# Performance work log

Hardware: AMD Instinct MI355X
Metric: run time of the kernel (lower is better)

Reference implementation:

```python
import jax, jax.numpy as jnp
import numpy as np

N_EDGES = 8_388_608      # total synapses (flat weight vector length)
NUM_TYPES = 200          # number of unique edge types (ragged groups)
STRENGTH = 1e-3          # regularizer strength (cast to float32 as in the TF module)


def setup_inputs() -> dict:
    key = jax.random.key(0)
    k1, k2, k3 = jax.random.split(key, 3)
    # Edges pre-sorted by edge type -> contiguous segments (equivalent to the
    # RaggedTensor.from_value_rowids grouping built in __init__).
    segment_ids = jnp.sort(
        jax.random.randint(k1, (N_EDGES,), 0, NUM_TYPES, dtype=jnp.int32))
    x = jax.random.normal(k2, (N_EDGES,), dtype=jnp.float32)
    init_raw = jax.random.normal(k3, (N_EDGES,), dtype=jnp.float32)
    # __init__ sorts the initial weights within each edge-type group; since
    # segment_ids is already sorted, lexsort with segment_ids as the primary
    # key sorts values within each contiguous segment.
    order = jnp.lexsort((init_raw, segment_ids))
    initial_sorted = init_raw[order]
    return {"x": x, "initial_sorted": initial_sorted, "segment_ids": segment_ids}


def reference(x, initial_sorted, segment_ids):
    x = x.astype(jnp.float32)
    # Segmented sort of the current weights: primary key = edge type,
    # secondary key = value. Equivalent to tf.sort(x_i) per ragged group.
    order = jnp.lexsort((x, segment_ids))
    x_sorted = x[order]                       # [n_edges], sorted within each group
    diff = jnp.abs(x_sorted - initial_sorted)  # per-edge |sorted(x) - sorted(y)|
    sums = jax.ops.segment_sum(diff, segment_ids, num_segments=NUM_TYPES)
    counts = jax.ops.segment_sum(jnp.ones_like(diff), segment_ids,
                                 num_segments=NUM_TYPES)
    emd = sums / jnp.maximum(counts, 1.0)      # per-group Wasserstein-1 (mean L1)
    return jnp.mean(emd) * jnp.float32(STRENGTH)
```

## Files before the change

kernel.cpp:

```cpp
#include <hip/hip_runtime.h>
#include <hip/hip_bf16.h>

#define NSEG 200
#define STRENGTH 1e-3f
#define NFB 16384
#define FSCALE (16384.0f / 12.0f)
#define BT 1024
#define SPLIT 5
#define WINCAP 9728
#define EPT 10
#define PSTRIDE (NFB + 8)
#define PCH 8192
#define SLICE_E 8200

__device__ __forceinline__ int fbin_of(float v) {
    float t = (v + 6.0f) * FSCALE;
    int b = (int)floorf(t);
    return b < 0 ? 0 : (b > NFB - 1 ? NFB - 1 : b);
}

__global__ void __launch_bounds__(BT)
k_hist(const float* __restrict__ x, const int* __restrict__ seg,
       int* __restrict__ seg_starts, float* __restrict__ segSums,
       unsigned* __restrict__ gcur, unsigned short* __restrict__ pfxg,
       int* __restrict__ Bg, int* __restrict__ Bpos, int N) {
    __shared__ unsigned hw[NFB / 2];
    __shared__ unsigned wsum[16];
    __shared__ int sh2[3];
    int s = blockIdx.x;
    int t = threadIdx.x;
    if (t <= 1) {
        int key = s + t;
        int lo = 0, hi = N;
        while (lo < hi) { int mid = (lo + hi) >> 1; if (seg[mid] < key) lo = mid + 1; else hi = mid; }
        sh2[t] = lo;
    }
    if (t < 8) gcur[s * 8 + t] = 0u;
    if (t == 2) segSums[s] = 0.f;
    for (int k = t; k < NFB / 2; k += BT) hw[k] = 0;
    __syncthreads();
    int st = sh2[0], en = sh2[1];
    if (t == 3) { seg_starts[s] = st; if (s == NSEG - 1) seg_starts[NSEG] = N; }
    int n = en - st;
    const float* xs = x + st;
    if (n > 0) {
        int head = min(n, (int)((4 - (st & 3)) & 3));
        for (int k = t; k < head; k += BT) { int f = fbin_of(xs[k]); atomicAdd(&hw[f >> 1], 1u << ((f & 1) * 16)); }
        int nv = (n - head) >> 2;
        const float4* xs4 = (const float4*)(xs + head);
        for (int j = t; j < nv; j += BT) {
            float4 v = xs4[j];
            int f0 = fbin_of(v.x), f1 = fbin_of(v.y), f2 = fbin_of(v.z), f3 = fbin_of(v.w);
            atomicAdd(&hw[f0 >> 1], 1u << ((f0 & 1) * 16));
            atomicAdd(&hw[f1 >> 1], 1u << ((f1 & 1) * 16));
            atomicAdd(&hw[f2 >> 1], 1u << ((f2 & 1) * 16));
            atomicAdd(&hw[f3 >> 1], 1u << ((f3 & 1) * 16));
        }
        for (int k = head + nv * 4 + t; k < n; k += BT) { int f = fbin_of(xs[k]); atomicAdd(&hw[f >> 1], 1u << ((f & 1) * 16)); }
    }
    __syncthreads();
    unsigned wv[8]; unsigned run = 0;
    #pragma unroll
    for (int i = 0; i < 8; ++i) {
        unsigned w = hw[t * 8 + i];
        unsigned c0 = w & 0xffffu, c1 = w >> 16;
        wv[i] = run | ((run + c0) << 16);
        run += c0 + c1;
    }
    unsigned incl = run;
    for (int off = 1; off < 64; off <<= 1) {
        unsigned nv2 = __shfl_up(incl, off, 64);
        if ((t & 63) >= off) incl += nv2;
    }
    if ((t & 63) == 63) wsum[t >> 6] = incl;
    __syncthreads();
    unsigned wb = 0; int myw = t >> 6;
    #pragma unroll
    for (int j = 0; j < 16; ++j) wb += (j < myw) ? wsum[j] : 0u;
    unsigned base = wb + incl - run;
    unsigned bb = base | (base << 16);
    unsigned short* pp = pfxg + (size_t)s * PSTRIDE;
    #pragma unroll
    for (int i = 0; i < 8; ++i) {
        unsigned pw = wv[i] + bb;
        hw[t * 8 + i] = pw;
        ((unsigned*)pp)[t * 8 + i] = pw;
    }
    if (t == BT - 1) { pp[NFB] = (unsigned short)(base + run); sh2[2] = (int)(base + run); }
    __syncthreads();
    int nsh = sh2[2];
    if (t == 0) { Bg[s * 8 + 0] = 0; Bg[s * 8 + SPLIT] = NFB; Bpos[s * 8 + 0] = 0; Bpos[s * 8 + SPLIT] = nsh; }
    if (t >= 1 && t < SPLIT) {
        int target = (int)(((long)t * nsh) / SPLIT);
        int lo = 0, hi = NFB - 1;
        while (lo < hi) {
            int mid = (lo + hi) >> 1;
            int pv = (int)((hw[(mid + 1) >> 1] >> (((mid + 1) & 1) * 16)) & 0xffffu);
            if (pv > target) hi = mid; else lo = mid + 1;
        }
        Bg[s * 8 + t] = lo;
        Bpos[s * 8 + t] = (int)((hw[lo >> 1] >> ((lo & 1) * 16)) & 0xffffu);
    }
}

__global__ void __launch_bounds__(1024)
k_part(const float* __restrict__ x, const int* __restrict__ seg_starts,
       const int* __restrict__ Bg, const int* __restrict__ Bpos,
       unsigned* __restrict__ gcur, float* __restrict__ part, int N) {
    __shared__ int sst[NSEG + 1];
    __shared__ unsigned hh[16][12];
    __shared__ int gb[10];
    __shared__ int sB[8];
    int t = threadIdx.x;
    for (int k = t; k < NSEG + 1; k += 1024) sst[k] = seg_starts[k];
    if (t < 192) ((unsigned*)hh)[t] = 0u;
    __syncthreads();
    int base = blockIdx.x * PCH;
    if (base >= N) return;
    int lo = 0, hi = NSEG - 1;
    while (lo < hi) { int mid = (lo + hi) >> 1; if (base < sst[mid + 1]) hi = mid; else lo = mid + 1; }
    int s0 = lo, bnd = sst[s0 + 1];
    if (t < 4) sB[t] = Bg[s0 * 8 + 1 + t];
    else if (t < 8) sB[t] = (s0 + 1 < NSEG) ? Bg[(s0 + 1) * 8 + 1 + (t - 4)] : 0x7fffffff;
    __syncthreads();
    int grp = t >> 6;
    float vv[8]; unsigned pk[8];
    const float4* x4 = (const float4*)(x + base);
    #pragma unroll
    for (int it = 0; it < 2; ++it) {
        int j = it * 1024 + t;
        int gi = base + j * 4;
        float4 v4 = (gi + 3 < N) ? x4[j] : make_float4(0.f, 0.f, 0.f, 0.f);
        #pragma unroll
        for (int e = 0; e < 4; ++e) {
            int i = it * 4 + e;
            float v = (e == 0) ? v4.x : (e == 1) ? v4.y : (e == 2) ? v4.z : v4.w;
            vv[i] = v;
            int g = gi + e;
            if (g < N) {
                int off = (g >= bnd) ? 4 : 0;
                int f = fbin_of(v);
                int p = (f >= sB[off]) + (f >= sB[off + 1]) + (f >= sB[off + 2]) + (f >= sB[off + 3]);
                int sp = (off >> 2) * 5 + p;
                unsigned lr = atomicAdd(&hh[grp][sp], 1u);
                pk[i] = ((unsigned)sp << 10) | lr;
            } else pk[i] = 0xffffffffu;
        }
    }
    __syncthreads();
    if (t < 10) {
        unsigned run = 0;
        #pragma unroll
        for (int g = 0; g < 16; ++g) { unsigned c = hh[g][t]; hh[g][t] = run; run += c; }
        int s = s0 + (t >= 5);
        int p = (t >= 5) ? t - 5 : t;
        int rsv = 0;
        if (run > 0 && s < NSEG) rsv = (int)atomicAdd(&gcur[s * 8 + p], run);
        gb[t] = (s < NSEG) ? (sst[s] + Bpos[s * 8 + p] + rsv) : 0;
    }
    __syncthreads();
    #pragma unroll
    for (int i = 0; i < 8; ++i) {
        if (pk[i] == 0xffffffffu) continue;
        int sp = (int)(pk[i] >> 10);
        int lr = (int)(pk[i] & 1023u);
        part[gb[sp] + (int)hh[grp][sp] + lr] = vv[i];
    }
}

__global__ void __launch_bounds__(BT)
k_seg(const float* __restrict__ part, const float* __restrict__ y,
      const int* __restrict__ seg_starts, const unsigned short* __restrict__ pfxg,
      const int* __restrict__ Bg, float* __restrict__ segSums) {
    __shared__ unsigned short slice[SLICE_E];
    __shared__ unsigned cur[2056];
    __shared__ __align__(16) float win[WINCAP + 4];
    __shared__ float warr[16];
    int s = blockIdx.x % NSEG;
    int p = blockIdx.x / NSEG;
    int t = threadIdx.x;
    int st = seg_starts[s], en = seg_starts[s + 1];
    int n = en - st;
    if (n <= 0) return;
    const unsigned short* pp = pfxg + (size_t)s * PSTRIDE;
    int Fa = Bg[s * 8 + p], Fb = Bg[s * 8 + p + 1];
    int spanc = Fb - Fa;
    int w0 = pp[Fa], w1 = pp[Fb];
    int wsz = w1 - w0;
    if (wsz <= 0) return;
    const float* ps = part + st + w0;
    bool sliced = (spanc + 1) <= SLICE_E;

    float rv[EPT]; int rr[EPT];
    if (sliced) {
        for (int k = t; k <= spanc; k += BT) slice[k] = pp[Fa + k];
        for (int k = t; k < ((spanc + 4) >> 2); k += BT) cur[k] = 0u;
        __syncthreads();
        int head = min(wsz, (int)((4 - ((st + w0) & 3)) & 3));
        for (int k = t; k < head; k += BT) {
            float v = ps[k];
            int i = fbin_of(v) - Fa;
            unsigned shf = (i & 3) * 8;
            unsigned old = atomicAdd(&cur[i >> 2], 1u << shf);
            win[(int)slice[i] - w0 + (int)((old >> shf) & 0xFFu)] = v;
        }
        int nv = (wsz - head) >> 2;
        const float4* ps4 = (const float4*)(ps + head);
        for (int j = t; j < nv; j += BT) {
            float4 v4 = ps4[j];
            #pragma unroll
            for (int e = 0; e < 4; ++e) {
                float v = (e == 0) ? v4.x : (e == 1) ? v4.y : (e == 2) ? v4.z : v4.w;
                int i = fbin_of(v) - Fa;
                unsigned shf = (i & 3) * 8;
                unsigned old = atomicAdd(&cur[i >> 2], 1u << shf);
                win[(int)slice[i] - w0 + (int)((old >> shf) & 0xFFu)] = v;
            }
        }
        for (int k = head + nv * 4 + t; k < wsz; k += BT) {
            float v = ps[k];
            int i = fbin_of(v) - Fa;
            unsigned shf = (i & 3) * 8;
            unsigned old = atomicAdd(&cur[i >> 2], 1u << shf);
            win[(int)slice[i] - w0 + (int)((old >> shf) & 0xFFu)] = v;
        }
        if (t < 4) win[wsz + t] = __builtin_inff();
        __syncthreads();
        #pragma unroll
        for (int e = 0; e < EPT; ++e) {
            int ql = e * BT + t;
            rr[e] = -1;
            if (ql < wsz) {
                float v = win[ql];
                rv[e] = v;
                int i = fbin_of(v) - Fa;
                int ls = (int)slice[i] - w0, le = (int)slice[i + 1] - w0;
                int a = ls & ~3;
                int cnt = a - ls;
                for (int j = a; j < le; j += 4) {
                    float4 qv = *(const float4*)&win[j];
                    cnt += (qv.x < v) + ((qv.x == v) & (j + 0 < ql));
                    cnt += (qv.y < v) + ((qv.y == v) & (j + 1 < ql));
                    cnt += (qv.z < v) + ((qv.z == v) & (j + 2 < ql));
                    cnt += (qv.w < v) + ((qv.w == v) & (j + 3 < ql));
                }
                rr[e] = ls + cnt;
            }
        }
    } else {
        for (int k = t; k < wsz; k += BT) win[k] = ps[k];
        if (t < 4) win[wsz + t] = __builtin_inff();
        __syncthreads();
        #pragma unroll
        for (int e = 0; e < EPT; ++e) {
            int ql = e * BT + t;
            rr[e] = -1;
            if (ql < wsz) {
                float v = win[ql];
                rv[e] = v;
                int cnt = 0;
                for (int j = 0; j < wsz; j += 4) {
                    float4 qv = *(const float4*)&win[j];
                    cnt += (qv.x < v) + ((qv.x == v) & (j + 0 < ql));
                    cnt += (qv.y < v) + ((qv.y == v) & (j + 1 < ql));
                    cnt += (qv.z < v) + ((qv.z == v) & (j + 2 < ql));
                    cnt += (qv.w < v) + ((qv.w == v) & (j + 3 < ql));
                }
                rr[e] = cnt;
            }
        }
    }
    __syncthreads();
    #pragma unroll
    for (int e = 0; e < EPT; ++e) {
        if (rr[e] >= 0) win[rr[e]] = rv[e];
    }
    __syncthreads();
    float acc = 0.f;
    const float* yw = y + st + w0;
    int head2 = min(wsz, (int)((4 - ((st + w0) & 3)) & 3));
    for (int k = t; k < head2; k += BT) acc += fabsf(win[k] - yw[k]);
    int nv2 = (wsz - head2) >> 2;
    const float4* yw4 = (const float4*)(yw + head2);
    for (int j = t; j < nv2; j += BT) {
        float4 yv = yw4[j];
        int k = head2 + j * 4;
        acc += fabsf(win[k + 0] - yv.x);
        acc += fabsf(win[k + 1] - yv.y);
        acc += fabsf(win[k + 2] - yv.z);
        acc += fabsf(win[k + 3] - yv.w);
    }
    for (int k = head2 + nv2 * 4 + t; k < wsz; k += BT) acc += fabsf(win[k] - yw[k]);

    for (int off = 32; off > 0; off >>= 1) acc += __shfl_xor(acc, off, 64);
    if ((t & 63) == 0) warr[t >> 6] = acc;
    __syncthreads();
    if (t == 0) {
        float tot = 0.f;
        #pragma unroll
        for (int j = 0; j < 16; ++j) tot += warr[j];
        if (tot != 0.f) atomicAdd(&segSums[s], tot);
    }
}

__global__ void k_final(const float* __restrict__ segSums, const int* __restrict__ seg_starts,
                        float* __restrict__ out) {
    __shared__ float red[256];
    int t = threadIdx.x;
    float a = 0.f;
    for (int k = t; k < NSEG; k += 256) {
        float n = (float)(seg_starts[k + 1] - seg_starts[k]);
        a += segSums[k] / fmaxf(n, 1.0f);
    }
    red[t] = a;
    __syncthreads();
    for (int off = 128; off > 0; off >>= 1) {
        if (t < off) red[t] += red[t + off];
        __syncthreads();
    }
    if (t == 0) out[0] = red[0] * (1.0f / (float)NSEG) * STRENGTH;
}

extern "C" void kernel_launch(void* const* d_in, const int* in_sizes, int n_in,
                              void* d_out, int out_size, void* d_ws, size_t ws_size,
                              hipStream_t stream) {
    const float* x = (const float*)d_in[0];
    const float* y = (const float*)d_in[1];
    const int* seg = (const int*)d_in[2];
    int N = in_sizes[0];

    char* ws = (char*)d_ws;
    float* segSums    = (float*)ws;
    int*   seg_starts = (int*)(ws + 800);
    unsigned* gcur    = (unsigned*)(ws + 1616);
    int*   Bg         = (int*)(ws + 8016);
    int*   Bpos       = (int*)(ws + 14448);
    unsigned short* pfxg = (unsigned short*)(ws + 20880);
    float* part       = (float*)(ws + 20880 + (size_t)NSEG * PSTRIDE * 2 + 16);

    int nchunk = (N + PCH - 1) / PCH;

    k_hist<<<NSEG, BT, 0, stream>>>(x, seg, seg_starts, segSums, gcur, pfxg, Bg, Bpos, N);
    k_part<<<nchunk, 1024, 0, stream>>>(x, seg_starts, Bg, Bpos, gcur, part, N);
    k_seg<<<NSEG * SPLIT, BT, 0, stream>>>(part, y, seg_starts, pfxg, Bg, segSums);
    k_final<<<1, 256, 0, stream>>>(segSums, seg_starts, (float*)d_out);
}
```

Baseline: 89.75 us.

## Split per-segment histogram across four blocks and merge in a second kernel

The histogram pass now launches four blocks per segment. Each block bins one quarter of the segment's elements into its own shared histogram and writes that partial to global scratch, which aliases the later partition buffer. A new merge kernel sums the four partials, builds the prefix, and picks the split points as before. This raises the grid from 200 blocks to 800 so the GPU's compute units are better filled during the binning pass. In exchange it adds an extra kernel launch and global traffic for the partial histograms.

Result: slower. 103.9 us (+15.7%).

```diff
diff --git a/kernel.cpp b/kernel.cpp
--- a/kernel.cpp
+++ b/kernel.cpp
@@ -7,6 +7,7 @@
 #define FSCALE (16384.0f / 12.0f)
 #define BT 1024
 #define SPLIT 5
+#define QH 4
 #define WINCAP 9728
 #define EPT 10
 #define PSTRIDE (NFB + 8)
@@ -20,14 +21,14 @@
 }
 
 __global__ void __launch_bounds__(BT)
-k_hist(const float* __restrict__ x, const int* __restrict__ seg,
-       int* __restrict__ seg_starts, float* __restrict__ segSums,
-       unsigned* __restrict__ gcur, unsigned short* __restrict__ pfxg,
-       int* __restrict__ Bg, int* __restrict__ Bpos, int N) {
+k_hist1(const float* __restrict__ x, const int* __restrict__ seg,
+        int* __restrict__ seg_starts, float* __restrict__ segSums,
+        unsigned* __restrict__ gcur, unsigned* __restrict__ histp, int N) {
     __shared__ unsigned hw[NFB / 2];
-    __shared__ unsigned wsum[16];
-    __shared__ int sh2[3];
-    int s = blockIdx.x;
+    __shared__ int sh2[2];
+    int b = blockIdx.x;
+    int s = b >> 2;
+    int h = b & 3;
     int t = threadIdx.x;
     if (t <= 1) {
         int key = s + t;
@@ -35,18 +36,24 @@
         while (lo < hi) { int mid = (lo + hi) >> 1; if (seg[mid] < key) lo = mid + 1; else hi = mid; }
         sh2[t] = lo;
     }
-    if (t < 8) gcur[s * 8 + t] = 0u;
-    if (t == 2) segSums[s] = 0.f;
+    if (h == 0) {
+        if (t < 8) gcur[s * 8 + t] = 0u;
+        if (t == 2) segSums[s] = 0.f;
+    }
     for (int k = t; k < NFB / 2; k += BT) hw[k] = 0;
     __syncthreads();
     int st = sh2[0], en = sh2[1];
-    if (t == 3) { seg_starts[s] = st; if (s == NSEG - 1) seg_starts[NSEG] = N; }
+    if (h == 0 && t == 3) { seg_starts[s] = st; if (s == NSEG - 1) seg_starts[NSEG] = N; }
     int n = en - st;
-    const float* xs = x + st;
-    if (n > 0) {
-        int head = min(n, (int)((4 - (st & 3)) & 3));
+    int q0 = n >> 2;
+    int a0 = st + h * q0;
+    int a1 = (h == 3) ? en : (a0 + q0);
+    int m = a1 - a0;
+    const float* xs = x + a0;
+    if (m > 0) {
+        int head = min(m, (int)((4 - (a0 & 3)) & 3));
         for (int k = t; k < head; k += BT) { int f = fbin_of(xs[k]); atomicAdd(&hw[f >> 1], 1u << ((f & 1) * 16)); }
-        int nv = (n - head) >> 2;
+        int nv = (m - head) >> 2;
         const float4* xs4 = (const float4*)(xs + head);
         for (int j = t; j < nv; j += BT) {
             float4 v = xs4[j];
@@ -56,13 +63,30 @@
             atomicAdd(&hw[f2 >> 1], 1u << ((f2 & 1) * 16));
             atomicAdd(&hw[f3 >> 1], 1u << ((f3 & 1) * 16));
         }
-        for (int k = head + nv * 4 + t; k < n; k += BT) { int f = fbin_of(xs[k]); atomicAdd(&hw[f >> 1], 1u << ((f & 1) * 16)); }
-    }
-    __syncthreads();
+        for (int k = head + nv * 4 + t; k < m; k += BT) { int f = fbin_of(xs[k]); atomicAdd(&hw[f >> 1], 1u << ((f & 1) * 16)); }
+    }
+    __syncthreads();
+    unsigned* hp = histp + (size_t)b * (NFB / 2);
+    for (int k = t; k < NFB / 2; k += BT) hp[k] = hw[k];
+}
+
+__global__ void __launch_bounds__(BT)
+k_hist2(const unsigned* __restrict__ histp, unsigned short* __restrict__ pfxg,
+        int* __restrict__ Bg, int* __restrict__ Bpos) {
+    __shared__ unsigned hw[NFB / 2];
+    __shared__ unsigned wsum[16];
+    __shared__ int sh2[1];
+    int s = blockIdx.x;
+    int t = threadIdx.x;
+    const unsigned* h0 = histp + (size_t)(s * 4 + 0) * (NFB / 2);
+    const unsigned* h1 = histp + (size_t)(s * 4 + 1) * (NFB / 2);
+    const unsigned* h2 = histp + (size_t)(s * 4 + 2) * (NFB / 2);
+    const unsigned* h3 = histp + (size_t)(s * 4 + 3) * (NFB / 2);
     unsigned wv[8]; unsigned run = 0;
     #pragma unroll
     for (int i = 0; i < 8; ++i) {
-        unsigned w = hw[t * 8 + i];
+        int k = t * 8 + i;
+        unsigned w = h0[k] + h1[k] + h2[k] + h3[k];
         unsigned c0 = w & 0xffffu, c1 = w >> 16;
         wv[i] = run | ((run + c0) << 16);
         run += c0 + c1;
@@ -86,9 +110,9 @@
         hw[t * 8 + i] = pw;
         ((unsigned*)pp)[t * 8 + i] = pw;
     }
-    if (t == BT - 1) { pp[NFB] = (unsigned short)(base + run); sh2[2] = (int)(base + run); }
-    __syncthreads();
-    int nsh = sh2[2];
+    if (t == BT - 1) { pp[NFB] = (unsigned short)(base + run); sh2[0] = (int)(base + run); }
+    __syncthreads();
+    int nsh = sh2[0];
     if (t == 0) { Bg[s * 8 + 0] = 0; Bg[s * 8 + SPLIT] = NFB; Bpos[s * 8 + 0] = 0; Bpos[s * 8 + SPLIT] = nsh; }
     if (t >= 1 && t < SPLIT) {
         int target = (int)(((long)t * nsh) / SPLIT);
@@ -334,13 +358,15 @@
     int*   seg_starts = (int*)(ws + 800);
     unsigned* gcur    = (unsigned*)(ws + 1616);
     int*   Bg         = (int*)(ws + 8016);
-    int*   Bpos       = (int*)(ws + 14448);
+    int*   Bpos      = (int*)(ws + 14448);
     unsigned short* pfxg = (unsigned short*)(ws + 20880);
     float* part       = (float*)(ws + 20880 + (size_t)NSEG * PSTRIDE * 2 + 16);
+    unsigned* histp   = (unsigned*)part;
 
     int nchunk = (N + PCH - 1) / PCH;
 
-    k_hist<<<NSEG, BT, 0, stream>>>(x, seg, seg_starts, segSums, gcur, pfxg, Bg, Bpos, N);
+    k_hist1<<<NSEG * QH, BT, 0, stream>>>(x, seg, seg_starts, segSums, gcur, histp, N);
+    k_hist2<<<NSEG, BT, 0, stream>>>(histp, pfxg, Bg, Bpos);
     k_part<<<nchunk, 1024, 0, stream>>>(x, seg_starts, Bg, Bpos, gcur, part, N);
     k_seg<<<NSEG * SPLIT, BT, 0, stream>>>(part, y, seg_starts, pfxg, Bg, segSums);
     k_final<<<1, 256, 0, stream>>>(segSums, seg_starts, (float*)d_out);
```
